# Kernel tuning notes

Hardware: AMD Instinct MI355X
Metric: run time of the kernel (lower is better)

## Reference

```python
import jax, jax.numpy as jnp
import numpy as np

CHAN = 128
IN_CHAN = 64
N_LAY = 4
N_OUT = 1000


def _affine_sample(img, theta):
    """F.affine_grid + F.grid_sample (bilinear, zeros padding, align_corners=False).
    img: [B, C, H, W]; theta: [C, 2, 3] (one affine per channel, shared over batch).
    """
    B, C, H, W = img.shape
    dt = img.dtype
    xs = (jnp.arange(W, dtype=dt) + 0.5) * (2.0 / W) - 1.0
    ys = (jnp.arange(H, dtype=dt) + 0.5) * (2.0 / H) - 1.0
    gx, gy = jnp.meshgrid(xs, ys)                      # [H, W] (xy indexing)
    base = jnp.stack([gx, gy, jnp.ones_like(gx)], -1)  # [H, W, 3]
    grid = jnp.einsum('cij,hwj->chwi', theta, base)    # [C, H, W, 2] (x, y)
    ix = ((grid[..., 0] + 1.0) * W - 1.0) * 0.5        # unnormalize, align_corners=False
    iy = ((grid[..., 1] + 1.0) * H - 1.0) * 0.5
    x0 = jnp.floor(ix)
    y0 = jnp.floor(iy)
    wx1 = ix - x0
    wy1 = iy - y0
    x0i = x0.astype(jnp.int32)
    y0i = y0.astype(jnp.int32)
    cidx = jnp.arange(C)[:, None, None]

    def tap(yi, xi, w):
        valid = (xi >= 0) & (xi < W) & (yi >= 0) & (yi < H)
        v = img[:, cidx, jnp.clip(yi, 0, H - 1), jnp.clip(xi, 0, W - 1)]  # [B,C,H,W]
        return v * (w * valid.astype(dt))[None]

    return (tap(y0i, x0i, (1 - wy1) * (1 - wx1))
            + tap(y0i, x0i + 1, (1 - wy1) * wx1)
            + tap(y0i + 1, x0i, wy1 * (1 - wx1))
            + tap(y0i + 1, x0i + 1, wy1 * wx1))


def _geom_layer(x, lin, geo, box):
    # expand-multiply-sum channel mix == einsum
    mixed = jnp.einsum('ci,bihw->bchw', lin, x)        # [B, chan, H, W]
    b = _affine_sample(jnp.ones_like(mixed), box)      # warped box of ones
    w = _affine_sample(mixed, geo)                     # warped features
    return w * b


def setup_inputs() -> dict:
    key = jax.random.key(0)
    ks = jax.random.split(key, 10)
    eye = jnp.eye(3, dtype=jnp.float32)[:2]            # [2, 3]
    x = jax.random.normal(ks[0], (16, IN_CHAN, 96, 96), dtype=jnp.float32)
    in_geo = eye[None] + 0.1 * jax.random.normal(ks[1], (CHAN, 2, 3), dtype=jnp.float32)
    in_box = eye[None] + 0.1 * jax.random.normal(ks[2], (CHAN, 2, 3), dtype=jnp.float32)
    in_lin = jax.random.uniform(ks[3], (CHAN, IN_CHAN), dtype=jnp.float32)
    lay_geo = eye[None, None] + 0.1 * jax.random.normal(ks[4], (N_LAY, CHAN, 2, 3), dtype=jnp.float32)
    lay_box = eye[None, None] + 0.1 * jax.random.normal(ks[5], (N_LAY, CHAN, 2, 3), dtype=jnp.float32)
    lay_lin = jax.random.uniform(ks[6], (N_LAY, CHAN, CHAN), dtype=jnp.float32)
    bound = 1.0 / np.sqrt(CHAN)
    dense_w = jax.random.uniform(ks[7], (N_OUT, CHAN), dtype=jnp.float32, minval=-bound, maxval=bound)
    dense_b = jax.random.uniform(ks[8], (N_OUT,), dtype=jnp.float32, minval=-bound, maxval=bound)
    return {"x": x, "in_geo": in_geo, "in_box": in_box, "in_lin": in_lin,
            "lay_geo": lay_geo, "lay_box": lay_box, "lay_lin": lay_lin,
            "dense_w": dense_w, "dense_b": dense_b}


def reference(x, in_geo, in_box, in_lin, lay_geo, lay_box, lay_lin, dense_w, dense_b):
    x = _geom_layer(x, in_lin, in_geo, in_box)
    for i in range(lay_lin.shape[0]):                  # resCon=True
        x = _geom_layer(x, lay_lin[i], lay_geo[i], lay_box[i]) + x
    feat_maps = x
    pooled = feat_maps.mean(axis=(-2, -1))             # [B, chan]
    logits = pooled @ dense_w.T + dense_b              # [B, nbOut]
    return (logits, feat_maps)
```

## Files before the change

### kernel.cpp

```cpp
#include <hip/hip_runtime.h>
#include <stdint.h>

#define HW 96
#define NPIX 9216
#define NCH 128
#define NB 16
#define HP 98

using bf16x8 = __attribute__((ext_vector_type(8))) short;
using f32x4  = __attribute__((ext_vector_type(4))) float;

__device__ inline uint32_t packbf(float v) {
    uint32_t u  = __float_as_uint(v);
    uint32_t rh = (u + 0x7FFFu + ((u >> 16) & 1u)) & 0xFFFF0000u;
    float    lo = v - __uint_as_float(rh);
    uint32_t ul = __float_as_uint(lo);
    uint32_t rl = ((ul + 0x7FFFu + ((ul >> 16) & 1u)) >> 16) & 0xFFFFu;
    return rh | rl;
}

__global__ __launch_bounds__(256) void packlin_kernel(const float* __restrict__ lin,
                                                      uint32_t* __restrict__ linP, int n) {
    const int i = blockIdx.x * 256 + threadIdx.x;
    if (i < n) linP[i] = packbf(lin[i]);
}

template<int K>
__global__ __launch_bounds__(512, 4) void mix_kernel(const float* __restrict__ x,
                                                     const float* __restrict__ lin,
                                                     float* __restrict__ mixed) {
    const int b    = blockIdx.y;
    const int lane = threadIdx.x & 63;
    const int p    = blockIdx.x * 128 + lane * 2;
    const int c0   = __builtin_amdgcn_readfirstlane((threadIdx.x >> 6) * 16);
    const float* xb = x + (size_t)b * K * NPIX + p;
    const float* lr = lin + c0 * K;

    float2 acc[16];
    #pragma unroll
    for (int c = 0; c < 16; ++c) acc[c] = float2{0.f, 0.f};

    for (int k0 = 0; k0 < K; k0 += 8) {
        float2 xv[8];
        #pragma unroll
        for (int j = 0; j < 8; ++j)
            xv[j] = *(const float2*)&xb[(size_t)(k0 + j) * NPIX];
        #pragma unroll
        for (int c = 0; c < 16; ++c) {
            const float* lc = lr + c * K + k0;
            #pragma unroll
            for (int j = 0; j < 8; ++j) {
                acc[c].x = fmaf(lc[j], xv[j].x, acc[c].x);
                acc[c].y = fmaf(lc[j], xv[j].y, acc[c].y);
            }
        }
    }
    float* ob = mixed + (size_t)b * NCH * NPIX + p;
    #pragma unroll
    for (int c = 0; c < 16; ++c)
        *(float2*)&ob[(size_t)(c0 + c) * NPIX] = acc[c];
}

__global__ __launch_bounds__(512, 2) void mix_mfma_kernel(const uint32_t* __restrict__ xP,
                                                          const uint32_t* __restrict__ lp,
                                                          float* __restrict__ mixed) {
    __shared__ uint32_t xs[128 * 128];
    const int b   = blockIdx.y;
    const int px0 = blockIdx.x * 128;
    const int t   = threadIdx.x;

    const uint32_t* xb = xP + (size_t)b * NCH * NPIX + px0;
    #pragma unroll
    for (int i = 0; i < 8; ++i) {
        const int f4  = i * 512 + t;
        const int row = f4 >> 5;
        const int c4  = (f4 & 31) << 2;
        const uint4 v = *(const uint4*)&xb[(size_t)row * NPIX + c4];
        uint32_t* d = &xs[row * 128 + (c4 ^ ((row & 0xC) << 2))];
        d[0] = v.x; d[1] = v.y; d[2] = v.z; d[3] = v.w;
    }

    const int l  = t & 63;
    const int wv = t >> 6;
    const int c0 = wv * 16;
    const int lq = l >> 4;
    const int lr = l & 15;

    bf16x8 AH[4], AL[4];
    const uint32_t* lrow = lp + (size_t)(c0 + lr) * NCH;
    #pragma unroll
    for (int q = 0; q < 4; ++q) {
        const uint4 a0 = *(const uint4*)&lrow[q * 32 + lq * 4];
        const uint4 a1 = *(const uint4*)&lrow[q * 32 + 16 + lq * 4];
        union { uint32_t w[4]; bf16x8 v; } h, m;
        h.w[0] = (a0.x >> 16) | (a0.y & 0xFFFF0000u);
        h.w[1] = (a0.z >> 16) | (a0.w & 0xFFFF0000u);
        h.w[2] = (a1.x >> 16) | (a1.y & 0xFFFF0000u);
        h.w[3] = (a1.z >> 16) | (a1.w & 0xFFFF0000u);
        m.w[0] = (a0.x & 0xFFFFu) | (a0.y << 16);
        m.w[1] = (a0.z & 0xFFFFu) | (a0.w << 16);
        m.w[2] = (a1.x & 0xFFFFu) | (a1.y << 16);
        m.w[3] = (a1.z & 0xFFFFu) | (a1.w << 16);
        AH[q] = h.v; AL[q] = m.v;
    }

    f32x4 acc[8];
    #pragma unroll
    for (int n = 0; n < 8; ++n) acc[n] = f32x4{0.f, 0.f, 0.f, 0.f};

    __syncthreads();

    const int pswz = lq << 4;
    #pragma unroll
    for (int q = 0; q < 4; ++q) {
        const int kb = q * 32 + lq * 4;
        #pragma unroll
        for (int np = 0; np < 4; ++np) {
            const int n0 = np * 2;
            bf16x8 BH0, BL0, BH1, BL1;
            #pragma unroll
            for (int s = 0; s < 2; ++s) {
                const int px = ((n0 + s) * 16 + lr) ^ pswz;
                const uint32_t u0 = xs[(kb + 0) * 128 + px];
                const uint32_t u1 = xs[(kb + 1) * 128 + px];
                const uint32_t u2 = xs[(kb + 2) * 128 + px];
                const uint32_t u3 = xs[(kb + 3) * 128 + px];
                const uint32_t u4 = xs[(kb + 16) * 128 + px];
                const uint32_t u5 = xs[(kb + 17) * 128 + px];
                const uint32_t u6 = xs[(kb + 18) * 128 + px];
                const uint32_t u7 = xs[(kb + 19) * 128 + px];
                union { uint32_t w[4]; bf16x8 v; } h, m;
                h.w[0] = (u0 >> 16) | (u1 & 0xFFFF0000u);
                h.w[1] = (u2 >> 16) | (u3 & 0xFFFF0000u);
                h.w[2] = (u4 >> 16) | (u5 & 0xFFFF0000u);
                h.w[3] = (u6 >> 16) | (u7 & 0xFFFF0000u);
                m.w[0] = (u0 & 0xFFFFu) | (u1 << 16);
                m.w[1] = (u2 & 0xFFFFu) | (u3 << 16);
                m.w[2] = (u4 & 0xFFFFu) | (u5 << 16);
                m.w[3] = (u6 & 0xFFFFu) | (u7 << 16);
                if (s == 0) { BH0 = h.v; BL0 = m.v; } else { BH1 = h.v; BL1 = m.v; }
            }
            acc[n0]     = __builtin_amdgcn_mfma_f32_16x16x32_bf16(AH[q], BH0, acc[n0],     0, 0, 0);
            acc[n0 + 1] = __builtin_amdgcn_mfma_f32_16x16x32_bf16(AH[q], BH1, acc[n0 + 1], 0, 0, 0);
            acc[n0]     = __builtin_amdgcn_mfma_f32_16x16x32_bf16(AH[q], BL0, acc[n0],     0, 0, 0);
            acc[n0 + 1] = __builtin_amdgcn_mfma_f32_16x16x32_bf16(AH[q], BL1, acc[n0 + 1], 0, 0, 0);
            acc[n0]     = __builtin_amdgcn_mfma_f32_16x16x32_bf16(AL[q], BH0, acc[n0],     0, 0, 0);
            acc[n0 + 1] = __builtin_amdgcn_mfma_f32_16x16x32_bf16(AL[q], BH1, acc[n0 + 1], 0, 0, 0);
            acc[n0]     = __builtin_amdgcn_mfma_f32_16x16x32_bf16(AL[q], BL0, acc[n0],     0, 0, 0);
            acc[n0 + 1] = __builtin_amdgcn_mfma_f32_16x16x32_bf16(AL[q], BL1, acc[n0 + 1], 0, 0, 0);
        }
    }

    float* ob = mixed + ((size_t)b * NCH + c0 + lq * 4) * NPIX + px0 + lr;
    #pragma unroll
    for (int n = 0; n < 8; ++n)
        #pragma unroll
        for (int r = 0; r < 4; ++r)
            ob[(size_t)r * NPIX + n * 16] = acc[n][r];
}

__device__ inline float clamp01(float z) { return fminf(fmaxf(z, 0.f), 1.f); }

template<bool RES, bool POOL, bool WRITEP>
__global__ __launch_bounds__(512) void sample_kernel(const float* __restrict__ mixed,
                                                     const float* __restrict__ geo,
                                                     const float* __restrict__ box,
                                                     float* __restrict__ out,
                                                     float* __restrict__ pooled,
                                                     uint32_t* xpw) {
    __shared__ float m[HP * HP];
    const int c = blockIdx.x;
    const int b = blockIdx.y;
    const int t = threadIdx.x;
    if (t < HP) {
        m[t] = 0.f;
        m[(HP - 1) * HP + t] = 0.f;
    } else if (t < HP + 96) {
        const int h = t - HP + 1;
        m[h * HP] = 0.f;
        m[h * HP + HP - 1] = 0.f;
    }
    const float* src = mixed + ((size_t)b * NCH + c) * NPIX;
    #pragma unroll
    for (int r = 0; r < NPIX / 512; ++r) {
        const int idx = r * 512 + t;
        const int h = idx / 96, w = idx - (idx / 96) * 96;
        m[(h + 1) * HP + (w + 1)] = src[idx];
    }
    const float* gth = geo + c * 6;
    const float* bth = box + c * 6;
    const float g0 = gth[0], g1 = gth[1], g3 = gth[3], g4 = gth[4];
    const float gcx = 48.f * gth[2] - 47.5f * (g0 + g1) + 47.5f;
    const float gcy = 48.f * gth[5] - 47.5f * (g3 + g4) + 47.5f;
    const float b0 = bth[0], b1 = bth[1], b3 = bth[3], b4 = bth[4];
    const float bcx = 48.f * bth[2] - 47.5f * (b0 + b1) + 47.5f;
    const float bcy = 48.f * bth[5] - 47.5f * (b3 + b4) + 47.5f;
    float* o = out + ((size_t)b * NCH + c) * NPIX;
    uint32_t* xp = xpw + ((size_t)b * NCH + c) * NPIX;
    __syncthreads();
    float psum = 0.f;
    #pragma unroll 6
    for (int r = 0; r < NPIX / 512; ++r) {
        const int p = r * 512 + t;
        const int h = p / 96, w = p - (p / 96) * 96;
        const float fw = (float)w, fh = (float)h;
        float ix = fmaf(g0, fw, fmaf(g1, fh, gcx));
        float iy = fmaf(g3, fw, fmaf(g4, fh, gcy));
        ix = fminf(fmaxf(ix, -1.f), 96.f);
        iy = fminf(fmaxf(iy, -1.f), 96.f);
        const float x0f = floorf(ix), y0f = floorf(iy);
        const float fx = ix - x0f, fy = iy - y0f;
        const int base = ((int)y0f + 1) * HP + ((int)x0f + 1);
        const float m00 = m[base],      m01 = m[base + 1];
        const float m10 = m[base + HP], m11 = m[base + HP + 1];
        const float mx0 = fmaf(fx, m01 - m00, m00);
        const float mx1 = fmaf(fx, m11 - m10, m10);
        float v = fmaf(fy, mx1 - mx0, mx0);
        const float bx = fmaf(b0, fw, fmaf(b1, fh, bcx));
        const float by = fmaf(b3, fw, fmaf(b4, fh, bcy));
        const float Xs = fminf(clamp01(bx + 1.f), clamp01(96.f - bx));
        const float Ys = fminf(clamp01(by + 1.f), clamp01(96.f - by));
        v *= Xs * Ys;
        if (RES) v += o[p];
        o[p] = v;
        if (WRITEP) xp[p] = packbf(v);
        if (POOL) psum += v;
    }
    if (POOL) {
        #pragma unroll
        for (int off = 32; off > 0; off >>= 1) psum += __shfl_down(psum, off, 64);
        __shared__ float red[8];
        if ((t & 63) == 0) red[t >> 6] = psum;
        __syncthreads();
        if (t == 0) {
            float s = 0.f;
            #pragma unroll
            for (int i = 0; i < 8; ++i) s += red[i];
            pooled[b * NCH + c] = s * (1.f / (float)NPIX);
        }
    }
}

__global__ __launch_bounds__(256) void pool_kernel(const float* __restrict__ feat,
                                                   float* __restrict__ pooled) {
    const int bc = blockIdx.x;
    const float4* f = (const float4*)(feat + (size_t)bc * NPIX);
    float s = 0.f;
    for (int i = threadIdx.x; i < NPIX / 4; i += 256) {
        const float4 v = f[i];
        s += (v.x + v.y) + (v.z + v.w);
    }
    #pragma unroll
    for (int off = 32; off > 0; off >>= 1) s += __shfl_down(s, off, 64);
    __shared__ float red[4];
    if ((threadIdx.x & 63) == 0) red[threadIdx.x >> 6] = s;
    __syncthreads();
    if (threadIdx.x == 0)
        pooled[bc] = (red[0] + red[1] + red[2] + red[3]) * (1.f / (float)NPIX);
}

__global__ __launch_bounds__(256) void dense_kernel(const float* __restrict__ pooled,
                                                    const float* __restrict__ Wt,
                                                    const float* __restrict__ bias,
                                                    float* __restrict__ out) {
    const int idx = blockIdx.x * 256 + threadIdx.x;
    if (idx >= NB * 1000) return;
    const int b = idx / 1000, n = idx - b * 1000;
    float acc = bias[n];
    const float* p = pooled + b * NCH;
    const float* wr = Wt + n * NCH;
    #pragma unroll 4
    for (int c = 0; c < NCH; ++c) acc = fmaf(p[c], wr[c], acc);
    out[idx] = acc;
}

extern "C" void kernel_launch(void* const* d_in, const int* in_sizes, int n_in,
                              void* d_out, int out_size, void* d_ws, size_t ws_size,
                              hipStream_t stream) {
    const float* x       = (const float*)d_in[0];
    const float* in_geo  = (const float*)d_in[1];
    const float* in_box  = (const float*)d_in[2];
    const float* in_lin  = (const float*)d_in[3];
    const float* lay_geo = (const float*)d_in[4];
    const float* lay_box = (const float*)d_in[5];
    const float* lay_lin = (const float*)d_in[6];
    const float* dense_w = (const float*)d_in[7];
    const float* dense_b = (const float*)d_in[8];

    float* out  = (float*)d_out;
    float* feat = out + NB * 1000;
    float* mixed = (float*)d_ws;

    const size_t mixedFloats = (size_t)NB * NCH * NPIX;
    const bool fusedPool = ws_size >= (mixedFloats + NB * NCH) * sizeof(float);
    const bool mfmaOK    = ws_size >= (mixedFloats + NB * NCH + 4 * NCH * NCH) * sizeof(float);
    float* pooled = fusedPool ? (float*)d_ws + mixedFloats : (float*)d_ws;

    const dim3 mixGrid(NPIX / 128, NB);
    const dim3 smpGrid(NCH, NB);

    if (mfmaOK) {
        uint32_t* xP   = (uint32_t*)d_ws;
        uint32_t* linP = (uint32_t*)((float*)d_ws + mixedFloats + NB * NCH);
        packlin_kernel<<<(4 * NCH * NCH + 255) / 256, 256, 0, stream>>>(lay_lin, linP, 4 * NCH * NCH);
        mix_kernel<64><<<mixGrid, 512, 0, stream>>>(x, in_lin, mixed);
        sample_kernel<false, false, true><<<smpGrid, 512, 0, stream>>>(mixed, in_geo, in_box, feat, pooled, xP);
        for (int i = 0; i < 3; ++i) {
            mix_mfma_kernel<<<mixGrid, 512, 0, stream>>>(xP, linP + (size_t)i * NCH * NCH, mixed);
            sample_kernel<true, false, true><<<smpGrid, 512, 0, stream>>>(mixed, lay_geo + i * NCH * 6,
                                                                          lay_box + i * NCH * 6, feat, pooled, xP);
        }
        mix_mfma_kernel<<<mixGrid, 512, 0, stream>>>(xP, linP + (size_t)3 * NCH * NCH, mixed);
        sample_kernel<true, true, false><<<smpGrid, 512, 0, stream>>>(mixed, lay_geo + 3 * NCH * 6,
                                                                      lay_box + 3 * NCH * 6, feat, pooled, xP);
    } else {
        uint32_t* dummy = (uint32_t*)d_ws;
        mix_kernel<64><<<mixGrid, 512, 0, stream>>>(x, in_lin, mixed);
        sample_kernel<false, false, false><<<smpGrid, 512, 0, stream>>>(mixed, in_geo, in_box, feat, pooled, dummy);
        for (int i = 0; i < 3; ++i) {
            mix_kernel<128><<<mixGrid, 512, 0, stream>>>(feat, lay_lin + i * NCH * NCH, mixed);
            sample_kernel<true, false, false><<<smpGrid, 512, 0, stream>>>(mixed, lay_geo + i * NCH * 6,
                                                                           lay_box + i * NCH * 6, feat, pooled, dummy);
        }
        mix_kernel<128><<<mixGrid, 512, 0, stream>>>(feat, lay_lin + 3 * NCH * NCH, mixed);
        if (fusedPool) {
            sample_kernel<true, true, false><<<smpGrid, 512, 0, stream>>>(mixed, lay_geo + 3 * NCH * 6,
                                                                          lay_box + 3 * NCH * 6, feat, pooled, dummy);
        } else {
            sample_kernel<true, false, false><<<smpGrid, 512, 0, stream>>>(mixed, lay_geo + 3 * NCH * 6,
                                                                           lay_box + 3 * NCH * 6, feat, pooled, dummy);
            pool_kernel<<<NB * NCH, 256, 0, stream>>>(feat, pooled);
        }
    }
    dense_kernel<<<(NB * 1000 + 255) / 256, 256, 0, stream>>>(pooled, dense_w, dense_b, out);
}
```

Before: 488.5 us.

## Pack fp32 to bf16 pairs inside MFMA mix kernel instead of writing packed copy

The sample kernel no longer writes a second packed hi/lo bf16 copy of each output. The MFMA mix kernel now reads fp32 features directly and splits them into bf16 pairs while loading into shared memory. The first layer's channel mix also moves from the scalar FMA kernel to a templated MFMA kernel with K=64, using a packed copy of in_lin. This removes a full-size extra write per layer and speeds up the first mix, at the cost of more packing arithmetic in the mix kernel's load phase.

```diff
diff --git a/kernel.cpp b/kernel.cpp
--- a/kernel.cpp
+++ b/kernel.cpp
@@ -61,23 +61,25 @@
         *(float2*)&ob[(size_t)(c0 + c) * NPIX] = acc[c];
 }
 
-__global__ __launch_bounds__(512, 2) void mix_mfma_kernel(const uint32_t* __restrict__ xP,
+template<int K>
+__global__ __launch_bounds__(512, 2) void mix_mfma_kernel(const float* __restrict__ xf,
                                                           const uint32_t* __restrict__ lp,
                                                           float* __restrict__ mixed) {
-    __shared__ uint32_t xs[128 * 128];
+    __shared__ uint32_t xs[K * 128];
     const int b   = blockIdx.y;
     const int px0 = blockIdx.x * 128;
     const int t   = threadIdx.x;
 
-    const uint32_t* xb = xP + (size_t)b * NCH * NPIX + px0;
-    #pragma unroll
-    for (int i = 0; i < 8; ++i) {
+    const float* xb = xf + (size_t)b * K * NPIX + px0;
+    #pragma unroll
+    for (int i = 0; i < K / 16; ++i) {
         const int f4  = i * 512 + t;
         const int row = f4 >> 5;
         const int c4  = (f4 & 31) << 2;
-        const uint4 v = *(const uint4*)&xb[(size_t)row * NPIX + c4];
-        uint32_t* d = &xs[row * 128 + (c4 ^ ((row & 0xC) << 2))];
-        d[0] = v.x; d[1] = v.y; d[2] = v.z; d[3] = v.w;
+        const float4 v = *(const float4*)&xb[(size_t)row * NPIX + c4];
+        uint4 pv;
+        pv.x = packbf(v.x); pv.y = packbf(v.y); pv.z = packbf(v.z); pv.w = packbf(v.w);
+        *(uint4*)&xs[row * 128 + (c4 ^ ((row & 0xC) << 2))] = pv;
     }
 
     const int l  = t & 63;
@@ -86,10 +88,11 @@
     const int lq = l >> 4;
     const int lr = l & 15;
 
-    bf16x8 AH[4], AL[4];
-    const uint32_t* lrow = lp + (size_t)(c0 + lr) * NCH;
-    #pragma unroll
-    for (int q = 0; q < 4; ++q) {
+    constexpr int NQ = K / 32;
+    bf16x8 AH[NQ], AL[NQ];
+    const uint32_t* lrow = lp + (size_t)(c0 + lr) * K;
+    #pragma unroll
+    for (int q = 0; q < NQ; ++q) {
         const uint4 a0 = *(const uint4*)&lrow[q * 32 + lq * 4];
         const uint4 a1 = *(const uint4*)&lrow[q * 32 + 16 + lq * 4];
         union { uint32_t w[4]; bf16x8 v; } h, m;
@@ -112,7 +115,7 @@
 
     const int pswz = lq << 4;
     #pragma unroll
-    for (int q = 0; q < 4; ++q) {
+    for (int q = 0; q < NQ; ++q) {
         const int kb = q * 32 + lq * 4;
         #pragma unroll
         for (int np = 0; np < 4; ++np) {
@@ -161,13 +164,12 @@
 
 __device__ inline float clamp01(float z) { return fminf(fmaxf(z, 0.f), 1.f); }
 
-template<bool RES, bool POOL, bool WRITEP>
+template<bool RES, bool POOL>
 __global__ __launch_bounds__(512) void sample_kernel(const float* __restrict__ mixed,
                                                      const float* __restrict__ geo,
                                                      const float* __restrict__ box,
                                                      float* __restrict__ out,
-                                                     float* __restrict__ pooled,
-                                                     uint32_t* xpw) {
+                                                     float* __restrict__ pooled) {
     __shared__ float m[HP * HP];
     const int c = blockIdx.x;
     const int b = blockIdx.y;
@@ -196,7 +198,6 @@
     const float bcx = 48.f * bth[2] - 47.5f * (b0 + b1) + 47.5f;
     const float bcy = 48.f * bth[5] - 47.5f * (b3 + b4) + 47.5f;
     float* o = out + ((size_t)b * NCH + c) * NPIX;
-    uint32_t* xp = xpw + ((size_t)b * NCH + c) * NPIX;
     __syncthreads();
     float psum = 0.f;
     #pragma unroll 6
@@ -223,7 +224,6 @@
         v *= Xs * Ys;
         if (RES) v += o[p];
         o[p] = v;
-        if (WRITEP) xp[p] = packbf(v);
         if (POOL) psum += v;
     }
     if (POOL) {
@@ -292,43 +292,44 @@
     float* mixed = (float*)d_ws;
 
     const size_t mixedFloats = (size_t)NB * NCH * NPIX;
+    const size_t linPWords   = 4 * NCH * NCH + NCH * 64;
     const bool fusedPool = ws_size >= (mixedFloats + NB * NCH) * sizeof(float);
-    const bool mfmaOK    = ws_size >= (mixedFloats + NB * NCH + 4 * NCH * NCH) * sizeof(float);
+    const bool mfmaOK    = ws_size >= (mixedFloats + NB * NCH + linPWords) * sizeof(float);
     float* pooled = fusedPool ? (float*)d_ws + mixedFloats : (float*)d_ws;
 
     const dim3 mixGrid(NPIX / 128, NB);
     const dim3 smpGrid(NCH, NB);
 
     if (mfmaOK) {
-        uint32_t* xP   = (uint32_t*)d_ws;
-        uint32_t* linP = (uint32_t*)((float*)d_ws + mixedFloats + NB * NCH);
+        uint32_t* linP  = (uint32_t*)((float*)d_ws + mixedFloats + NB * NCH);
+        uint32_t* linP0 = linP + 4 * NCH * NCH;
         packlin_kernel<<<(4 * NCH * NCH + 255) / 256, 256, 0, stream>>>(lay_lin, linP, 4 * NCH * NCH);
+        packlin_kernel<<<(NCH * 64 + 255) / 256, 256, 0, stream>>>(in_lin, linP0, NCH * 64);
+        mix_mfma_kernel<64><<<mixGrid, 512, 0, stream>>>(x, linP0, mixed);
+        sample_kernel<false, false><<<smpGrid, 512, 0, stream>>>(mixed, in_geo, in_box, feat, pooled);
+        for (int i = 0; i < 3; ++i) {
+            mix_mfma_kernel<128><<<mixGrid, 512, 0, stream>>>(feat, linP + (size_t)i * NCH * NCH, mixed);
+            sample_kernel<true, false><<<smpGrid, 512, 0, stream>>>(mixed, lay_geo + i * NCH * 6,
+                                                                    lay_box + i * NCH * 6, feat, pooled);
+        }
+        mix_mfma_kernel<128><<<mixGrid, 512, 0, stream>>>(feat, linP + (size_t)3 * NCH * NCH, mixed);
+        sample_kernel<true, true><<<smpGrid, 512, 0, stream>>>(mixed, lay_geo + 3 * NCH * 6,
+                                                               lay_box + 3 * NCH * 6, feat, pooled);
+    } else {
         mix_kernel<64><<<mixGrid, 512, 0, stream>>>(x, in_lin, mixed);
-        sample_kernel<false, false, true><<<smpGrid, 512, 0, stream>>>(mixed, in_geo, in_box, feat, pooled, xP);
-        for (int i = 0; i < 3; ++i) {
-            mix_mfma_kernel<<<mixGrid, 512, 0, stream>>>(xP, linP + (size_t)i * NCH * NCH, mixed);
-            sample_kernel<true, false, true><<<smpGrid, 512, 0, stream>>>(mixed, lay_geo + i * NCH * 6,
-                                                                          lay_box + i * NCH * 6, feat, pooled, xP);
-        }
-        mix_mfma_kernel<<<mixGrid, 512, 0, stream>>>(xP, linP + (size_t)3 * NCH * NCH, mixed);
-        sample_kernel<true, true, false><<<smpGrid, 512, 0, stream>>>(mixed, lay_geo + 3 * NCH * 6,
-                                                                      lay_box + 3 * NCH * 6, feat, pooled, xP);
-    } else {
-        uint32_t* dummy = (uint32_t*)d_ws;
-        mix_kernel<64><<<mixGrid, 512, 0, stream>>>(x, in_lin, mixed);
-        sample_kernel<false, false, false><<<smpGrid, 512, 0, stream>>>(mixed, in_geo, in_box, feat, pooled, dummy);
+        sample_kernel<false, false><<<smpGrid, 512, 0, stream>>>(mixed, in_geo, in_box, feat, pooled);
         for (int i = 0; i < 3; ++i) {
             mix_kernel<128><<<mixGrid, 512, 0, stream>>>(feat, lay_lin + i * NCH * NCH, mixed);
-            sample_kernel<true, false, false><<<smpGrid, 512, 0, stream>>>(mixed, lay_geo + i * NCH * 6,
-                                                                           lay_box + i * NCH * 6, feat, pooled, dummy);
+            sample_kernel<true, false><<<smpGrid, 512, 0, stream>>>(mixed, lay_geo + i * NCH * 6,
+                                                                    lay_box + i * NCH * 6, feat, pooled);
         }
         mix_kernel<128><<<mixGrid, 512, 0, stream>>>(feat, lay_lin + 3 * NCH * NCH, mixed);
         if (fusedPool) {
-            sample_kernel<true, true, false><<<smpGrid, 512, 0, stream>>>(mixed, lay_geo + 3 * NCH * 6,
-                                                                          lay_box + 3 * NCH * 6, feat, pooled, dummy);
+            sample_kernel<true, true><<<smpGrid, 512, 0, stream>>>(mixed, lay_geo + 3 * NCH * 6,
+                                                                   lay_box + 3 * NCH * 6, feat, pooled);
         } else {
-            sample_kernel<true, false, false><<<smpGrid, 512, 0, stream>>>(mixed, lay_geo + 3 * NCH * 6,
-                                                                           lay_box + 3 * NCH * 6, feat, pooled, dummy);
+            sample_kernel<true, false><<<smpGrid, 512, 0, stream>>>(mixed, lay_geo + 3 * NCH * 6,
+                                                                    lay_box + 3 * NCH * 6, feat, pooled);
             pool_kernel<<<NB * NCH, 256, 0, stream>>>(feat, pooled);
         }
     }
```

Measured after the change: 482.7 us. No clear change (-1.2%).
